# Kernel tuning notes

Measured on AMD Instinct MI355X. Metric: run time of the kernel, lower is better.

## Reference

```python
import jax, jax.numpy as jnp
import numpy as np

N_NODES = 100000
N_EDGES = 1600000
IN_C, HID_C, OUT_C = 128, 128, 64


def gcn_conv(x, src, dst, n_nodes, W, b):
    # PyG GCNConv (normalize=True, add_self_loops=True):
    # out = D^{-1/2} (A+I) D^{-1/2} (x @ W^T) + b
    h = x @ W.T                                   # [N, out]
    deg = jax.ops.segment_sum(jnp.ones(src.shape, x.dtype), dst,
                              num_segments=n_nodes)  # includes self-loops
    dinv = jnp.where(deg > 0, jax.lax.rsqrt(deg), 0.0)
    norm = dinv[src] * dinv[dst]                  # [E+N]
    msg = h[src] * norm[:, None]                  # gather + scale
    out = jax.ops.segment_sum(msg, dst, num_segments=n_nodes)
    return out + b


def setup_inputs() -> dict:
    key = jax.random.key(0)
    ks = jax.random.split(key, 8)
    x = jax.random.normal(ks[0], (N_NODES, IN_C), dtype=jnp.float32)
    edge_index = jax.random.randint(ks[1], (2, N_EDGES), 0, N_NODES, dtype=jnp.int64)

    def lin(k, fan_out, fan_in):
        s = 1.0 / np.sqrt(fan_in)
        kw, kb = jax.random.split(k)
        W = jax.random.uniform(kw, (fan_out, fan_in), jnp.float32, -s, s)
        b = jax.random.uniform(kb, (fan_out,), jnp.float32, -s, s)
        return W, b

    W1, b1 = lin(ks[2], HID_C, IN_C)
    W2, b2 = lin(ks[3], HID_C, HID_C)
    W3, b3 = lin(ks[4], OUT_C, HID_C)
    return {"x": x, "edge_index": edge_index,
            "W1": W1, "b1": b1, "W2": W2, "b2": b2, "W3": W3, "b3": b3}


def reference(x, edge_index, W1, b1, W2, b2, W3, b3):
    n = x.shape[0]
    loop = jnp.arange(n, dtype=edge_index.dtype)
    src = jnp.concatenate([edge_index[0], loop])  # add self-loops once; identical per layer
    dst = jnp.concatenate([edge_index[1], loop])
    h = gcn_conv(x, src, dst, n, W1, b1)
    h = jax.nn.relu(h)
    h = gcn_conv(h, src, dst, n, W2, b2)
    h = jax.nn.relu(h)
    h = gcn_conv(h, src, dst, n, W3, b3)
    return h
```

## Files before the change

kernel.cpp:

```cpp
#include <hip/hip_runtime.h>


#define NPB 256
#define CAP 4672
#define BIN_WGS 128

typedef short bfrag __attribute__((ext_vector_type(8)));
typedef float f32x4 __attribute__((ext_vector_type(4)));
typedef unsigned short u16x8 __attribute__((ext_vector_type(8)));

__global__ __launch_bounds__(256) void init_cur(int* __restrict__ cur, int B) {
  int i = blockIdx.x * 256 + threadIdx.x;
  if (i < B) cur[i] = i * CAP;
}

__global__ __launch_bounds__(256) void bin_edges(const int* __restrict__ src,
                                                 const int* __restrict__ dst,
                                                 int* __restrict__ cur,
                                                 int* __restrict__ binned,
                                                 int E, int B) {
  __shared__ int lc[512];
  __shared__ int lbase[512];
  const int t = threadIdx.x;
  const int chunk = (E + BIN_WGS - 1) / BIN_WGS;
  const int e0 = blockIdx.x * chunk;
  const int e1 = min(E, e0 + chunk);

  for (int i = t; i < B; i += 256) lc[i] = 0;
  __syncthreads();
  for (int e = e0 + t; e < e1; e += 256) {
    int d = dst[e];
    atomicAdd(&lc[d >> 8], 1);
  }
  __syncthreads();
  for (int i = t; i < B; i += 256) {
    int c = lc[i];
    lbase[i] = c ? atomicAdd(&cur[i], c) : 0;
    lc[i] = 0;
  }
  __syncthreads();
  for (int e = e0 + t; e < e1; e += 256) {
    int d = dst[e];
    int s = __builtin_nontemporal_load(&src[e]);
    int bk = d >> 8;
    int p = lbase[bk] + atomicAdd(&lc[bk], 1);
    if (p < (bk + 1) * CAP)
      binned[p] = ((d & 255) << 24) | s;
  }
}

__global__ __launch_bounds__(256) void build_buckets(const int* __restrict__ binned,
                                                     const int* __restrict__ cur,
                                                     int* __restrict__ cols,
                                                     int2* __restrict__ off2,
                                                     float* __restrict__ dinv,
                                                     int N) {
  __shared__ int eb[CAP];
  __shared__ int ob[CAP];
  __shared__ int lc[256];
  __shared__ int sc[256];
  const int b = blockIdx.x;
  const int t = threadIdx.x;
  const int base = b * CAP;
  const int cntb = min(cur[b] - base, CAP);

  for (int i = t; i < cntb; i += 256) eb[i] = binned[base + i];
  lc[t] = 0;
  __syncthreads();
  for (int i = t; i < cntb; i += 256)
    atomicAdd(&lc[(unsigned)eb[i] >> 24], 1);
  __syncthreads();
  int myc = lc[t];
  sc[t] = myc;
  __syncthreads();
  for (int d = 1; d < 256; d <<= 1) {
    int a = (t >= d) ? sc[t - d] : 0;
    __syncthreads();
    sc[t] += a;
    __syncthreads();
  }
  int excl = sc[t] - myc;
  int node = b * NPB + t;
  if (node < N) {
    off2[node] = make_int2(base + excl, base + excl + myc);
    dinv[node] = rsqrtf((float)(myc + 1));
  }
  lc[t] = excl;
  __syncthreads();
  for (int i = t; i < cntb; i += 256) {
    int e = eb[i];
    int p = atomicAdd(&lc[(unsigned)e >> 24], 1);
    ob[p] = e & 0xFFFFFF;
  }
  __syncthreads();
  for (int i = t; i < cntb; i += 256) cols[base + i] = ob[i];
}

__device__ inline unsigned short bf16rne(float x) {
  unsigned u = __float_as_uint(x);
  return (unsigned short)((u + 0x7FFFu + ((u >> 16) & 1u)) >> 16);
}
__device__ inline float bf16lo(unsigned q) { return __uint_as_float(q << 16); }
__device__ inline float bf16hi(unsigned q) { return __uint_as_float(q & 0xFFFF0000u); }

__global__ __launch_bounds__(256) void split_w(const float* __restrict__ W,
                                               unsigned short* __restrict__ hi,
                                               unsigned short* __restrict__ lo,
                                               int total) {
  int i = blockIdx.x * 256 + threadIdx.x;
  if (i < total) {
    float v = W[i];
    unsigned short h = bf16rne(v);
    hi[i] = h;
    lo[i] = bf16rne(v - __uint_as_float((unsigned)h << 16));
  }
}

#define LDP 136
template <int OUTC>
__global__ __launch_bounds__(256) void gemm_xw_mfma(const float* __restrict__ X,
                                                    const unsigned short* __restrict__ Whg,
                                                    const unsigned short* __restrict__ Wlg,
                                                    const float* __restrict__ dinv,
                                                    unsigned short* __restrict__ Y,
                                                    int M) {
  __shared__ unsigned short Xhi[64 * LDP], Xlo[64 * LDP];
  __shared__ unsigned short Whi[64 * LDP], Wlo[64 * LDP];
  const int tid = threadIdx.x;
  const int m_base = blockIdx.x * 64;

  for (int idx = tid; idx < 64 * 16; idx += 256) {
    int r = idx >> 4, g = idx & 15;
    int m = m_base + r;
    float4 v0 = make_float4(0.f, 0.f, 0.f, 0.f), v1 = v0;
    if (m < M) {
      const float4* px = (const float4*)(X + (size_t)m * 128 + g * 8);
      v0 = px[0];
      v1 = px[1];
    }
    float vv[8] = {v0.x, v0.y, v0.z, v0.w, v1.x, v1.y, v1.z, v1.w};
    u16x8 hv, lv;
#pragma unroll
    for (int j = 0; j < 8; ++j) {
      unsigned short h = bf16rne(vv[j]);
      float res = vv[j] - __uint_as_float((unsigned)h << 16);
      hv[j] = h;
      lv[j] = bf16rne(res);
    }
    *(u16x8*)(Xhi + r * LDP + g * 8) = hv;
    *(u16x8*)(Xlo + r * LDP + g * 8) = lv;
  }

  const int lane = tid & 63;
  const int wv = tid >> 6;
  const int col_l = lane & 15;
  const int quad = lane >> 4;
  const int aBase = (wv * 16 + col_l) * LDP + quad * 8;
  const int bBase = col_l * LDP + quad * 8;

  for (int cc = 0; cc < OUTC; cc += 64) {
    __syncthreads();
    for (int idx = tid; idx < 64 * 16; idx += 256) {
      int r = idx >> 4, g = idx & 15;
      u16x8 hv = *(const u16x8*)(Whg + (size_t)(cc + r) * 128 + g * 8);
      u16x8 lv = *(const u16x8*)(Wlg + (size_t)(cc + r) * 128 + g * 8);
      *(u16x8*)(Whi + r * LDP + g * 8) = hv;
      *(u16x8*)(Wlo + r * LDP + g * 8) = lv;
    }
    __syncthreads();

    f32x4 acc[4] = {{0.f, 0.f, 0.f, 0.f},
                    {0.f, 0.f, 0.f, 0.f},
                    {0.f, 0.f, 0.f, 0.f},
                    {0.f, 0.f, 0.f, 0.f}};
#pragma unroll
    for (int ks = 0; ks < 4; ++ks) {
      int ao = aBase + ks * 32;
      bfrag aHi = *(const bfrag*)(Xhi + ao);
      bfrag aLo = *(const bfrag*)(Xlo + ao);
#pragma unroll
      for (int t = 0; t < 4; ++t) {
        int bo = bBase + t * 16 * LDP + ks * 32;
        bfrag bHi = *(const bfrag*)(Whi + bo);
        bfrag bLo = *(const bfrag*)(Wlo + bo);
        acc[t] = __builtin_amdgcn_mfma_f32_16x16x32_bf16(aHi, bHi, acc[t], 0, 0, 0);
        acc[t] = __builtin_amdgcn_mfma_f32_16x16x32_bf16(aLo, bHi, acc[t], 0, 0, 0);
        acc[t] = __builtin_amdgcn_mfma_f32_16x16x32_bf16(aHi, bLo, acc[t], 0, 0, 0);
      }
    }

#pragma unroll
    for (int r = 0; r < 4; ++r) {
      int row = m_base + wv * 16 + quad * 4 + r;
      if (row < M) {
        float s = dinv[row];
#pragma unroll
        for (int t = 0; t < 4; ++t) {
          unsigned short h = bf16rne(acc[t][r] * s);
          Y[(size_t)row * OUTC + cc + t * 16 + col_l] = h;
        }
      }
    }
  }
}

template <int C, bool RELU>
__global__ __launch_bounds__(256) void aggregate2(const unsigned short* __restrict__ xs,
                                                  const int2* __restrict__ off2,
                                                  const int* __restrict__ cols,
                                                  const float* __restrict__ dinv,
                                                  const float* __restrict__ bias,
                                                  float* __restrict__ out, int N) {
  constexpr int CG = C / 8;
  constexpr int EG = 64 / CG;
  int wid = (int)((blockIdx.x * blockDim.x + threadIdx.x) >> 6);
  int lane = threadIdx.x & 63;
  if (wid >= N) return;
  const int eg = lane / CG;
  const int cg = lane % CG;

  float acc[8] = {0.f, 0.f, 0.f, 0.f, 0.f, 0.f, 0.f, 0.f};
  if (eg == 0) {
    uint4 d = *(const uint4*)(xs + (size_t)wid * C + cg * 8);
    acc[0] = bf16lo(d.x); acc[1] = bf16hi(d.x);
    acc[2] = bf16lo(d.y); acc[3] = bf16hi(d.y);
    acc[4] = bf16lo(d.z); acc[5] = bf16hi(d.z);
    acc[6] = bf16lo(d.w); acc[7] = bf16hi(d.w);
  }

  int2 oo = off2[wid];
  int ebase = oo.x;
  const int eend = oo.y;
  while (ebase < eend) {
    int cnt = eend - ebase;
    if (cnt > 64) cnt = 64;
    int col = (lane < cnt) ? __builtin_nontemporal_load(&cols[ebase + lane]) : 0;
    const int c1 = cnt - 1;
    for (int j = 0; j < cnt; j += 4 * EG) {
      int i0 = j + eg, i1 = i0 + EG, i2 = i1 + EG, i3 = i2 + EG;
      int s0 = __shfl(col, min(i0, c1));
      int s1 = __shfl(col, min(i1, c1));
      int s2 = __shfl(col, min(i2, c1));
      int s3 = __shfl(col, min(i3, c1));
      uint4 d0 = *(const uint4*)(xs + (size_t)s0 * C + cg * 8);
      uint4 d1 = *(const uint4*)(xs + (size_t)s1 * C + cg * 8);
      uint4 d2 = *(const uint4*)(xs + (size_t)s2 * C + cg * 8);
      uint4 d3 = *(const uint4*)(xs + (size_t)s3 * C + cg * 8);
      if (i0 < cnt) {
        acc[0] += bf16lo(d0.x); acc[1] += bf16hi(d0.x);
        acc[2] += bf16lo(d0.y); acc[3] += bf16hi(d0.y);
        acc[4] += bf16lo(d0.z); acc[5] += bf16hi(d0.z);
        acc[6] += bf16lo(d0.w); acc[7] += bf16hi(d0.w);
      }
      if (i1 < cnt) {
        acc[0] += bf16lo(d1.x); acc[1] += bf16hi(d1.x);
        acc[2] += bf16lo(d1.y); acc[3] += bf16hi(d1.y);
        acc[4] += bf16lo(d1.z); acc[5] += bf16hi(d1.z);
        acc[6] += bf16lo(d1.w); acc[7] += bf16hi(d1.w);
      }
      if (i2 < cnt) {
        acc[0] += bf16lo(d2.x); acc[1] += bf16hi(d2.x);
        acc[2] += bf16lo(d2.y); acc[3] += bf16hi(d2.y);
        acc[4] += bf16lo(d2.z); acc[5] += bf16hi(d2.z);
        acc[6] += bf16lo(d2.w); acc[7] += bf16hi(d2.w);
      }
      if (i3 < cnt) {
        acc[0] += bf16lo(d3.x); acc[1] += bf16hi(d3.x);
        acc[2] += bf16lo(d3.y); acc[3] += bf16hi(d3.y);
        acc[4] += bf16lo(d3.z); acc[5] += bf16hi(d3.z);
        acc[6] += bf16lo(d3.w); acc[7] += bf16hi(d3.w);
      }
    }
    ebase += cnt;
  }

#pragma unroll
  for (int m = CG; m < 64; m <<= 1) {
#pragma unroll
    for (int q = 0; q < 8; ++q) acc[q] += __shfl_xor(acc[q], m);
  }

  if (eg == 0) {
    float dd = dinv[wid];
    const float4 bA = *(const float4*)(bias + cg * 8);
    const float4 bB = *(const float4*)(bias + cg * 8 + 4);
    f32x4 oA, oB;
    oA[0] = acc[0] * dd + bA.x; oA[1] = acc[1] * dd + bA.y;
    oA[2] = acc[2] * dd + bA.z; oA[3] = acc[3] * dd + bA.w;
    oB[0] = acc[4] * dd + bB.x; oB[1] = acc[5] * dd + bB.y;
    oB[2] = acc[6] * dd + bB.z; oB[3] = acc[7] * dd + bB.w;
    if (RELU) {
#pragma unroll
      for (int q = 0; q < 4; ++q) {
        oA[q] = fmaxf(oA[q], 0.f);
        oB[q] = fmaxf(oB[q], 0.f);
      }
    }
    __builtin_nontemporal_store(oA, (f32x4*)(out + (size_t)wid * C + cg * 8));
    __builtin_nontemporal_store(oB, (f32x4*)(out + (size_t)wid * C + cg * 8 + 4));
  }
}


extern "C" void kernel_launch(void* const* d_in, const int* in_sizes, int n_in,
                              void* d_out, int out_size, void* d_ws, size_t ws_size,
                              hipStream_t stream) {
  const float* x  = (const float*)d_in[0];
  const int*   ei = (const int*)d_in[1];
  const float* W1 = (const float*)d_in[2];
  const float* b1 = (const float*)d_in[3];
  const float* W2 = (const float*)d_in[4];
  const float* b2 = (const float*)d_in[5];
  const float* W3 = (const float*)d_in[6];
  const float* b3 = (const float*)d_in[7];

  const int N = in_sizes[0] / 128;
  const int E = in_sizes[1] / 2;
  const int* src = ei;
  const int* dst = ei + E;
  const int B = (N + NPB - 1) / NPB;

  char* w = (char*)d_ws;
  size_t p = 0;
  auto alloc = [&](size_t bytes) -> void* {
    void* r = w + p;
    p = (p + bytes + 255) & ~(size_t)255;
    return r;
  };
  float*    dinv   = (float*)alloc((size_t)N * 4);
  int2*     off2   = (int2*)alloc((size_t)N * 8);
  int*      cur    = (int*)alloc((size_t)B * 4);
  int*      binned = (int*)alloc((size_t)B * CAP * 4);
  int*      cols   = (int*)alloc((size_t)B * CAP * 4);
  unsigned short* xsb = (unsigned short*)alloc((size_t)N * 128 * 2);
  float*    bufB   = (float*)alloc((size_t)N * 128 * 4);
  unsigned short* w1h = (unsigned short*)alloc(128 * 128 * 2);
  unsigned short* w1l = (unsigned short*)alloc(128 * 128 * 2);
  unsigned short* w2h = (unsigned short*)alloc(128 * 128 * 2);
  unsigned short* w2l = (unsigned short*)alloc(128 * 128 * 2);
  unsigned short* w3h = (unsigned short*)alloc(64 * 128 * 2);
  unsigned short* w3l = (unsigned short*)alloc(64 * 128 * 2);

  init_cur<<<(B + 255) / 256, 256, 0, stream>>>(cur, B);
  bin_edges<<<BIN_WGS, 256, 0, stream>>>(src, dst, cur, binned, E, B);
  split_w<<<64, 256, 0, stream>>>(W1, w1h, w1l, 128 * 128);
  split_w<<<64, 256, 0, stream>>>(W2, w2h, w2l, 128 * 128);
  split_w<<<32, 256, 0, stream>>>(W3, w3h, w3l, 64 * 128);
  build_buckets<<<B, 256, 0, stream>>>(binned, cur, cols, off2, dinv, N);

  const int gb = (N + 63) / 64;
  const int ab = (N + 3) / 4;

  gemm_xw_mfma<128><<<gb, 256, 0, stream>>>(x, w1h, w1l, dinv, xsb, N);
  aggregate2<128, true><<<ab, 256, 0, stream>>>(xsb, off2, cols, dinv, b1, bufB, N);
  gemm_xw_mfma<128><<<gb, 256, 0, stream>>>(bufB, w2h, w2l, dinv, xsb, N);
  aggregate2<128, true><<<ab, 256, 0, stream>>>(xsb, off2, cols, dinv, b2, bufB, N);
  gemm_xw_mfma<64><<<gb, 256, 0, stream>>>(bufB, w3h, w3l, dinv, xsb, N);
  aggregate2<64, false><<<ab, 256, 0, stream>>>(xsb, off2, cols, dinv, b3,
                                                (float*)d_out, N);
}
```

Baseline: 443.6 us.

## Read GEMM weight fragments from global memory, merge weight splits, widen binning grid

Result: slower. 480.8 us (+8.4%).

```diff
diff --git a/kernel.cpp b/kernel.cpp
--- a/kernel.cpp
+++ b/kernel.cpp
@@ -3,7 +3,7 @@
 
 #define NPB 256
 #define CAP 4672
-#define BIN_WGS 128
+#define BIN_WGS 512
 
 typedef short bfrag __attribute__((ext_vector_type(8)));
 typedef float f32x4 __attribute__((ext_vector_type(4)));
@@ -103,17 +103,32 @@
 __device__ inline float bf16lo(unsigned q) { return __uint_as_float(q << 16); }
 __device__ inline float bf16hi(unsigned q) { return __uint_as_float(q & 0xFFFF0000u); }
 
-__global__ __launch_bounds__(256) void split_w(const float* __restrict__ W,
-                                               unsigned short* __restrict__ hi,
-                                               unsigned short* __restrict__ lo,
-                                               int total) {
+__global__ __launch_bounds__(256) void split_w3(const float* __restrict__ W1,
+                                                const float* __restrict__ W2,
+                                                const float* __restrict__ W3,
+                                                unsigned short* __restrict__ w1h,
+                                                unsigned short* __restrict__ w1l,
+                                                unsigned short* __restrict__ w2h,
+                                                unsigned short* __restrict__ w2l,
+                                                unsigned short* __restrict__ w3h,
+                                                unsigned short* __restrict__ w3l) {
   int i = blockIdx.x * 256 + threadIdx.x;
-  if (i < total) {
-    float v = W[i];
-    unsigned short h = bf16rne(v);
-    hi[i] = h;
-    lo[i] = bf16rne(v - __uint_as_float((unsigned)h << 16));
-  }
+  const float* W;
+  unsigned short *hi, *lo;
+  int j;
+  if (i < 16384) {
+    W = W1; hi = w1h; lo = w1l; j = i;
+  } else if (i < 32768) {
+    W = W2; hi = w2h; lo = w2l; j = i - 16384;
+  } else if (i < 40960) {
+    W = W3; hi = w3h; lo = w3l; j = i - 32768;
+  } else {
+    return;
+  }
+  float v = W[j];
+  unsigned short h = bf16rne(v);
+  hi[j] = h;
+  lo[j] = bf16rne(v - __uint_as_float((unsigned)h << 16));
 }
 
 #define LDP 136
@@ -125,7 +140,6 @@
                                                     unsigned short* __restrict__ Y,
                                                     int M) {
   __shared__ unsigned short Xhi[64 * LDP], Xlo[64 * LDP];
-  __shared__ unsigned short Whi[64 * LDP], Wlo[64 * LDP];
   const int tid = threadIdx.x;
   const int m_base = blockIdx.x * 64;
 
@@ -150,25 +164,15 @@
     *(u16x8*)(Xhi + r * LDP + g * 8) = hv;
     *(u16x8*)(Xlo + r * LDP + g * 8) = lv;
   }
+  __syncthreads();
 
   const int lane = tid & 63;
   const int wv = tid >> 6;
   const int col_l = lane & 15;
   const int quad = lane >> 4;
   const int aBase = (wv * 16 + col_l) * LDP + quad * 8;
-  const int bBase = col_l * LDP + quad * 8;
 
   for (int cc = 0; cc < OUTC; cc += 64) {
-    __syncthreads();
-    for (int idx = tid; idx < 64 * 16; idx += 256) {
-      int r = idx >> 4, g = idx & 15;
-      u16x8 hv = *(const u16x8*)(Whg + (size_t)(cc + r) * 128 + g * 8);
-      u16x8 lv = *(const u16x8*)(Wlg + (size_t)(cc + r) * 128 + g * 8);
-      *(u16x8*)(Whi + r * LDP + g * 8) = hv;
-      *(u16x8*)(Wlo + r * LDP + g * 8) = lv;
-    }
-    __syncthreads();
-
     f32x4 acc[4] = {{0.f, 0.f, 0.f, 0.f},
                     {0.f, 0.f, 0.f, 0.f},
                     {0.f, 0.f, 0.f, 0.f},
@@ -180,9 +184,9 @@
       bfrag aLo = *(const bfrag*)(Xlo + ao);
 #pragma unroll
       for (int t = 0; t < 4; ++t) {
-        int bo = bBase + t * 16 * LDP + ks * 32;
-        bfrag bHi = *(const bfrag*)(Whi + bo);
-        bfrag bLo = *(const bfrag*)(Wlo + bo);
+        size_t wo = (size_t)(cc + t * 16 + col_l) * 128 + ks * 32 + quad * 8;
+        bfrag bHi = *(const bfrag*)(Whg + wo);
+        bfrag bLo = *(const bfrag*)(Wlg + wo);
         acc[t] = __builtin_amdgcn_mfma_f32_16x16x32_bf16(aHi, bHi, acc[t], 0, 0, 0);
         acc[t] = __builtin_amdgcn_mfma_f32_16x16x32_bf16(aLo, bHi, acc[t], 0, 0, 0);
         acc[t] = __builtin_amdgcn_mfma_f32_16x16x32_bf16(aHi, bLo, acc[t], 0, 0, 0);
@@ -343,9 +347,7 @@
 
   init_cur<<<(B + 255) / 256, 256, 0, stream>>>(cur, B);
   bin_edges<<<BIN_WGS, 256, 0, stream>>>(src, dst, cur, binned, E, B);
-  split_w<<<64, 256, 0, stream>>>(W1, w1h, w1l, 128 * 128);
-  split_w<<<64, 256, 0, stream>>>(W2, w2h, w2l, 128 * 128);
-  split_w<<<32, 256, 0, stream>>>(W3, w3h, w3l, 64 * 128);
+  split_w3<<<160, 256, 0, stream>>>(W1, W2, W3, w1h, w1l, w2h, w2l, w3h, w3l);
   build_buckets<<<B, 256, 0, stream>>>(binned, cur, cols, off2, dinv, N);
 
   const int gb = (N + 63) / 64;
```
